# Performance work log

Measured on AMD Instinct MI355X. Metric: run time of the kernel, lower is better.

## Reference

```python
import jax, jax.numpy as jnp
import numpy as np

EPS = 1e-6

def setup_inputs() -> dict:
    key = jax.random.key(0)
    k1, k2, k3 = jax.random.split(key, 3)
    N, L, S, H, D = 4, 4096, 4096, 8, 64
    queries = jax.random.normal(k1, (N, L, H, D), dtype=jnp.float32)
    keys = jax.random.normal(k2, (N, S, H, D), dtype=jnp.float32)
    values = jax.random.normal(k3, (N, S, H, D), dtype=jnp.float32)
    return {"queries": queries, "keys": keys, "values": values}

def _feature_map(x):
    # elu(x) + 1
    return jax.nn.elu(x) + 1.0

def reference(queries, keys, values):
    Q = _feature_map(queries)          # [N, L, H, D]
    K = _feature_map(keys)             # [N, S, H, D]
    v_length = values.shape[1]
    v = values / v_length              # [N, S, H, Dv]
    # KV outer-product sum over source positions: [N, H, D, Dv]
    KV = jnp.einsum('nshd,nshv->nhdv', K, v)
    # Normalizer: Q . sum_s K  -> [N, L, H]
    Z = 1.0 / (jnp.einsum('nlhd,nhd->nlh', Q, K.sum(axis=1)) + EPS)
    # Queried values: [N, L, H, Dv]
    out = jnp.einsum('nlhd,nhdv,nlh->nlhv', Q, KV, Z) * v_length
    return out
```

## Files before the change

kernel.cpp:

```cpp
#include <hip/hip_runtime.h>
#include <stdint.h>

#define NB   4
#define LQ   4096
#define SK   4096
#define NHD  8
#define DD   64
#define ROWSTRIDE (NHD * DD)
#define CH   16
#define SROWS (SK / CH)
#define KVSZ (DD * DD)
#define PART_STRIDE (KVSZ + DD)
#define NHTOT (NB * NHD)
#define LT   64
#define EPSF 1e-6f

typedef __attribute__((ext_vector_type(8))) short bf16x8;
typedef __attribute__((ext_vector_type(4))) float f32x4;

union FragU { uint32_t u[4]; bf16x8 v; };

__device__ __forceinline__ float fmap(float x) {
    return x > 0.f ? x + 1.f : __expf(x);
}

__device__ __forceinline__ void split8(const float* x, bf16x8& hi, bf16x8& lo) {
    FragU H, L;
#pragma unroll
    for (int p = 0; p < 4; ++p) {
        float a = x[2*p], b = x[2*p+1];
        uint32_t ua = __float_as_uint(a), ub = __float_as_uint(b);
        float ra = a - __uint_as_float(ua & 0xFFFF0000u);
        float rb = b - __uint_as_float(ub & 0xFFFF0000u);
        H.u[p] = (ua >> 16) | (ub & 0xFFFF0000u);
        L.u[p] = (__float_as_uint(ra) >> 16) | (__float_as_uint(rb) & 0xFFFF0000u);
    }
    hi = H.v; lo = L.v;
}

__global__ __launch_bounds__(256) void k1_kv(const float* __restrict__ Kin,
                                             const float* __restrict__ Vin,
                                             float* __restrict__ part) {
    const int blk   = blockIdx.x;
    const int nh    = blk / CH;
    const int chunk = blk % CH;
    const int n = nh / NHD, h = nh % NHD;
    const int t = threadIdx.x;
    const int w = t >> 6, lane = t & 63;
    const int g = lane >> 4, r = lane & 15;
    const int wm = w & 1, wn = w >> 1;

    const size_t base = ((size_t)n * SK + (size_t)chunk * SROWS) * ROWSTRIDE
                        + (size_t)h * DD;

    const f32x4 zero4 = {0.f, 0.f, 0.f, 0.f};
    f32x4 acc[2][2] = {{zero4, zero4}, {zero4, zero4}};
    float ks[2] = {0.f, 0.f};

    for (int s0 = 0; s0 < SROWS; s0 += 32) {
        float xa[2][8], xb[2][8];
#pragma unroll
        for (int i = 0; i < 8; ++i) {
            const int soff = ((i & 4) << 2) + 4 * g + (i & 3);
            const size_t rowb = base + (size_t)(s0 + soff) * ROWSTRIDE;
#pragma unroll
            for (int mt = 0; mt < 2; ++mt)
                xa[mt][i] = Kin[rowb + (wm*2 + mt)*16 + r];
#pragma unroll
            for (int nt = 0; nt < 2; ++nt)
                xb[nt][i] = Vin[rowb + (wn*2 + nt)*16 + r];
        }
        bf16x8 ahi[2], alo[2], bhi[2], blo[2];
#pragma unroll
        for (int mt = 0; mt < 2; ++mt) {
#pragma unroll
            for (int i = 0; i < 8; ++i) xa[mt][i] = fmap(xa[mt][i]);
            if (wn == 0) {
#pragma unroll
                for (int i = 0; i < 8; ++i) ks[mt] += xa[mt][i];
            }
            split8(xa[mt], ahi[mt], alo[mt]);
        }
#pragma unroll
        for (int nt = 0; nt < 2; ++nt) split8(xb[nt], bhi[nt], blo[nt]);
#pragma unroll
        for (int mt = 0; mt < 2; ++mt)
#pragma unroll
            for (int nt = 0; nt < 2; ++nt) {
                acc[mt][nt] = __builtin_amdgcn_mfma_f32_16x16x32_bf16(
                                  ahi[mt], bhi[nt], acc[mt][nt], 0, 0, 0);
                acc[mt][nt] = __builtin_amdgcn_mfma_f32_16x16x32_bf16(
                                  alo[mt], bhi[nt], acc[mt][nt], 0, 0, 0);
                acc[mt][nt] = __builtin_amdgcn_mfma_f32_16x16x32_bf16(
                                  ahi[mt], blo[nt], acc[mt][nt], 0, 0, 0);
            }
    }

    float* pb = part + ((size_t)nh * CH + chunk) * PART_STRIDE;
#pragma unroll
    for (int mt = 0; mt < 2; ++mt) {
        const int dbase = (wm*2 + mt)*16 + 4*g;
#pragma unroll
        for (int nt = 0; nt < 2; ++nt) {
            const int e = (wn*2 + nt)*16 + r;
#pragma unroll
            for (int j = 0; j < 4; ++j)
                pb[(dbase + j) * DD + e] = acc[mt][nt][j];
        }
    }
    if (wn == 0) {
#pragma unroll
        for (int mt = 0; mt < 2; ++mt) {
            float v = ks[mt];
            v += __shfl_xor(v, 16);
            v += __shfl_xor(v, 32);
            if (lane < 16) pb[KVSZ + (wm*2 + mt)*16 + lane] = v;
        }
    }
}

__global__ __launch_bounds__(256) void k2_reduce(const float* __restrict__ part,
                                                 float* __restrict__ fin) {
    const int idx = blockIdx.x * 256 + threadIdx.x;
    if (idx >= NHTOT * PART_STRIDE) return;
    const int nh = idx / PART_STRIDE;
    const int j  = idx - nh * PART_STRIDE;
    const float* p = part + (size_t)nh * CH * PART_STRIDE + j;
    float s = 0.f;
#pragma unroll
    for (int cix = 0; cix < CH; ++cix) s += p[(size_t)cix * PART_STRIDE];
    fin[idx] = s;
}

#define KVSTR 72

__global__ __launch_bounds__(256) void k3_out(const float* __restrict__ Qin,
                                              const float* __restrict__ fin,
                                              float* __restrict__ out) {
    const int blk = blockIdx.x;
    const int nh  = blk >> 6;
    const int lc  = blk & 63;
    const int n = nh >> 3, h = nh & 7;
    const int t = threadIdx.x;
    const int w = t >> 6, lane = t & 63;
    const int g = lane >> 4, r = lane & 15;

    __shared__ __align__(16) short KThi[DD][KVSTR];
    __shared__ __align__(16) short KTlo[DD][KVSTR];
    __shared__ __align__(16) float Ksm[DD];

    const float* fb = fin + (size_t)nh * PART_STRIDE;
    {
        const int e  = t & 63;
        const int dq = t >> 6;
#pragma unroll
        for (int dd = 0; dd < 16; ++dd) {
            const int d = dq * 16 + dd;
            const float x = fb[d * DD + e];
            const int col = (((d & 32) | (d & 3) | (((d >> 4) & 1) << 2)
                              | (((d >> 2) & 3) << 3)) ^ ((e & 3) << 3));
            const uint32_t ux = __float_as_uint(x);
            const float lo = x - __uint_as_float(ux & 0xFFFF0000u);
            KThi[e][col] = (short)(ux >> 16);
            KTlo[e][col] = (short)(__float_as_uint(lo) >> 16);
        }
        if (t < DD) Ksm[t] = fb[KVSZ + t];
    }
    __syncthreads();

    const size_t qrow = (size_t)n * LQ + (size_t)lc * LT + w * 16 + r;
    const float* qp = Qin + qrow * ROWSTRIDE + (size_t)h * DD;

    const f32x4 zero4 = {0.f, 0.f, 0.f, 0.f};
    f32x4 acc[4] = {zero4, zero4, zero4, zero4};
    float z = 0.f;

#pragma unroll
    for (int kst = 0; kst < 2; ++kst) {
        const int kb = kst * 32;
        const float4 qa = *(const float4*)(qp + kb + 4*g);
        const float4 qb = *(const float4*)(qp + kb + 16 + 4*g);
        float qv[8] = {fmap(qa.x), fmap(qa.y), fmap(qa.z), fmap(qa.w),
                       fmap(qb.x), fmap(qb.y), fmap(qb.z), fmap(qb.w)};
        const float4 ka = *(const float4*)&Ksm[kb + 4*g];
        const float4 kc = *(const float4*)&Ksm[kb + 16 + 4*g];
        z += qv[0]*ka.x + qv[1]*ka.y + qv[2]*ka.z + qv[3]*ka.w
           + qv[4]*kc.x + qv[5]*kc.y + qv[6]*kc.z + qv[7]*kc.w;
        bf16x8 ahi, alo;
        split8(qv, ahi, alo);
        const int cswz = 8 * (g ^ (r & 3));
#pragma unroll
        for (int nt = 0; nt < 4; ++nt) {
            const int e = nt*16 + r;
            const bf16x8 bh = *(const bf16x8*)&KThi[e][kb + cswz];
            const bf16x8 bl = *(const bf16x8*)&KTlo[e][kb + cswz];
            acc[nt] = __builtin_amdgcn_mfma_f32_16x16x32_bf16(ahi, bh, acc[nt], 0,0,0);
            acc[nt] = __builtin_amdgcn_mfma_f32_16x16x32_bf16(alo, bh, acc[nt], 0,0,0);
            acc[nt] = __builtin_amdgcn_mfma_f32_16x16x32_bf16(ahi, bl, acc[nt], 0,0,0);
        }
    }

    z += __shfl_xor(z, 16);
    z += __shfl_xor(z, 32);

    const size_t obase0 = ((size_t)n * LQ + (size_t)lc * LT + w * 16) * ROWSTRIDE
                          + (size_t)h * DD;
#pragma unroll
    for (int j = 0; j < 4; ++j) {
        const float zj = __shfl(z, 4*g + j);
        const float zi = 1.f / (zj + EPSF);
        const size_t ob = obase0 + (size_t)(4*g + j) * ROWSTRIDE;
#pragma unroll
        for (int nt = 0; nt < 4; ++nt)
            out[ob + nt*16 + r] = acc[nt][j] * zi;
    }
}

extern "C" void kernel_launch(void* const* d_in, const int* in_sizes, int n_in,
                              void* d_out, int out_size, void* d_ws, size_t ws_size,
                              hipStream_t stream) {
    const float* Q = (const float*)d_in[0];
    const float* K = (const float*)d_in[1];
    const float* V = (const float*)d_in[2];
    float* out = (float*)d_out;

    float* ws   = (float*)d_ws;
    float* part = ws;
    float* fin  = ws + (size_t)NHTOT * CH * PART_STRIDE;

    k1_kv<<<NHTOT * CH, 256, 0, stream>>>(K, V, part);
    k2_reduce<<<(NHTOT * PART_STRIDE + 255) / 256, 256, 0, stream>>>(part, fin);
    k3_out<<<NHTOT * (LQ / LT), 256, 0, stream>>>(Q, fin, out);
}
```

Before: 142.1 us.

## Double-buffer K/V loads in KV kernel and enlarge output tiles

The KV accumulation kernel now uses twice as many source chunks, so each block covers 128 rows. Its loop is unrolled into a software pipeline that issues the next tile's global loads before computing the current one, which hides load latency. The output kernel now processes 128 query rows per 512-thread block, and it loads the KV matrix with vectorized float4 reads, amortizing the shared-memory setup over more rows. The cost is higher register pressure in k1, more partials for the reduce kernel to sum, and fewer blocks in k3.

```diff
diff --git a/kernel.cpp b/kernel.cpp
--- a/kernel.cpp
+++ b/kernel.cpp
@@ -7,12 +7,12 @@
 #define NHD  8
 #define DD   64
 #define ROWSTRIDE (NHD * DD)
-#define CH   16
+#define CH   32
 #define SROWS (SK / CH)
 #define KVSZ (DD * DD)
 #define PART_STRIDE (KVSZ + DD)
 #define NHTOT (NB * NHD)
-#define LT   64
+#define LT   128
 #define EPSF 1e-6f
 
 typedef __attribute__((ext_vector_type(8))) short bf16x8;
@@ -57,32 +57,37 @@
     f32x4 acc[2][2] = {{zero4, zero4}, {zero4, zero4}};
     float ks[2] = {0.f, 0.f};
 
-    for (int s0 = 0; s0 < SROWS; s0 += 32) {
-        float xa[2][8], xb[2][8];
+    float A0[2][8], B0[2][8], A1[2][8], B1[2][8];
+
+    auto LOADT = [&](float (&XA)[2][8], float (&XB)[2][8], int s0) {
 #pragma unroll
         for (int i = 0; i < 8; ++i) {
             const int soff = ((i & 4) << 2) + 4 * g + (i & 3);
             const size_t rowb = base + (size_t)(s0 + soff) * ROWSTRIDE;
 #pragma unroll
             for (int mt = 0; mt < 2; ++mt)
-                xa[mt][i] = Kin[rowb + (wm*2 + mt)*16 + r];
+                XA[mt][i] = Kin[rowb + (wm*2 + mt)*16 + r];
 #pragma unroll
             for (int nt = 0; nt < 2; ++nt)
-                xb[nt][i] = Vin[rowb + (wn*2 + nt)*16 + r];
-        }
+                XB[nt][i] = Vin[rowb + (wn*2 + nt)*16 + r];
+        }
+    };
+
+    auto COMPUTE = [&](float (&XA)[2][8], float (&XB)[2][8]) {
         bf16x8 ahi[2], alo[2], bhi[2], blo[2];
 #pragma unroll
         for (int mt = 0; mt < 2; ++mt) {
-#pragma unroll
-            for (int i = 0; i < 8; ++i) xa[mt][i] = fmap(xa[mt][i]);
+            float xf[8];
+#pragma unroll
+            for (int i = 0; i < 8; ++i) xf[i] = fmap(XA[mt][i]);
             if (wn == 0) {
 #pragma unroll
-                for (int i = 0; i < 8; ++i) ks[mt] += xa[mt][i];
+                for (int i = 0; i < 8; ++i) ks[mt] += xf[i];
             }
-            split8(xa[mt], ahi[mt], alo[mt]);
-        }
-#pragma unroll
-        for (int nt = 0; nt < 2; ++nt) split8(xb[nt], bhi[nt], blo[nt]);
+            split8(xf, ahi[mt], alo[mt]);
+        }
+#pragma unroll
+        for (int nt = 0; nt < 2; ++nt) split8(XB[nt], bhi[nt], blo[nt]);
 #pragma unroll
         for (int mt = 0; mt < 2; ++mt)
 #pragma unroll
@@ -94,7 +99,13 @@
                 acc[mt][nt] = __builtin_amdgcn_mfma_f32_16x16x32_bf16(
                                   ahi[mt], blo[nt], acc[mt][nt], 0, 0, 0);
             }
-    }
+    };
+
+    LOADT(A0, B0, 0);
+    LOADT(A1, B1, 32);  COMPUTE(A0, B0);
+    LOADT(A0, B0, 64);  COMPUTE(A1, B1);
+    LOADT(A1, B1, 96);  COMPUTE(A0, B0);
+    COMPUTE(A1, B1);
 
     float* pb = part + ((size_t)nh * CH + chunk) * PART_STRIDE;
 #pragma unroll
@@ -134,12 +145,12 @@
 
 #define KVSTR 72
 
-__global__ __launch_bounds__(256) void k3_out(const float* __restrict__ Qin,
+__global__ __launch_bounds__(512) void k3_out(const float* __restrict__ Qin,
                                               const float* __restrict__ fin,
                                               float* __restrict__ out) {
     const int blk = blockIdx.x;
-    const int nh  = blk >> 6;
-    const int lc  = blk & 63;
+    const int nh  = blk >> 5;
+    const int lc  = blk & 31;
     const int n = nh >> 3, h = nh & 7;
     const int t = threadIdx.x;
     const int w = t >> 6, lane = t & 63;
@@ -151,14 +162,19 @@
 
     const float* fb = fin + (size_t)nh * PART_STRIDE;
     {
-        const int e  = t & 63;
-        const int dq = t >> 6;
-#pragma unroll
-        for (int dd = 0; dd < 16; ++dd) {
-            const int d = dq * 16 + dd;
-            const float x = fb[d * DD + e];
-            const int col = (((d & 32) | (d & 3) | (((d >> 4) & 1) << 2)
-                              | (((d >> 2) & 3) << 3)) ^ ((e & 3) << 3));
+        const int i0 = t * 8;
+        const int d  = i0 >> 6;
+        const int e0 = i0 & 63;
+        const float4 xa = *(const float4*)(fb + i0);
+        const float4 xb = *(const float4*)(fb + i0 + 4);
+        const float xs[8] = {xa.x, xa.y, xa.z, xa.w, xb.x, xb.y, xb.z, xb.w};
+        const int colb = (d & 32) | (d & 3) | (((d >> 4) & 1) << 2)
+                         | (((d >> 2) & 3) << 3);
+#pragma unroll
+        for (int m = 0; m < 8; ++m) {
+            const int e = e0 + m;
+            const int col = colb ^ ((e & 3) << 3);
+            const float x = xs[m];
             const uint32_t ux = __float_as_uint(x);
             const float lo = x - __uint_as_float(ux & 0xFFFF0000u);
             KThi[e][col] = (short)(ux >> 16);
@@ -230,5 +246,5 @@
 
     k1_kv<<<NHTOT * CH, 256, 0, stream>>>(K, V, part);
     k2_reduce<<<(NHTOT * PART_STRIDE + 255) / 256, 256, 0, stream>>>(part, fin);
-    k3_out<<<NHTOT * (LQ / LT), 256, 0, stream>>>(Q, fin, out);
-}
+    k3_out<<<NHTOT * (LQ / LT), 512, 0, stream>>>(Q, fin, out);
+}
```

Result: slower. 146.5 us (+3.1%).
